# Optimization experiments

Hardware: AMD Instinct MI355X
Metric: run time of the kernel (lower is better)

Reference implementation:

```python
import jax, jax.numpy as jnp
import numpy as np

NTOKEN = 32000
NHID = 1024
BATCH = 64
LEAVES = 256          # leaves per balanced binary tree
SEQLEN = 768          # 3*LEAVES-2 = 766, padded to 768
MAX_DEPTH = 64        # stack bound; balanced tree needs ~log2(LEAVES)+2
OPEN, CLOSE = 0, 1
PAD = NTOKEN - 1


def _build_tree(rng, n_leaves):
    # "( left right )" encoding: open, subtrees, close; leaf ids in [2, NTOKEN-2]
    if n_leaves == 1:
        return [int(rng.integers(2, NTOKEN - 1))]
    l = n_leaves // 2
    return [OPEN] + _build_tree(rng, l) + _build_tree(rng, n_leaves - l) + [CLOSE]


def setup_inputs() -> dict:
    rng = np.random.default_rng(0)
    seqs = []
    for _ in range(BATCH):
        s = _build_tree(rng, LEAVES)
        s = s + [PAD] * (SEQLEN - len(s))
        seqs.append(s)
    tokens = jnp.asarray(np.asarray(seqs, dtype=np.int32).T)  # [S, B]

    key = jax.random.key(0)
    k1, k2 = jax.random.split(key, 2)
    emb = jax.random.normal(k1, (NTOKEN, NHID), jnp.float32) * 0.1
    emb = emb.at[PAD].set(0.0)  # padding_idx row is zero
    W = jax.random.normal(k2, (NHID, 2 * NHID), jnp.float32) * (1.0 / np.sqrt(2 * NHID))
    b = jnp.zeros((NHID,), jnp.float32)
    return {"tokens": tokens, "emb": emb, "W": W, "b": b}


def _parse_all(tokens, emb, W, b):
    # tokens: [S, B] int32. Shift-reduce stack machine, scanned over sequence,
    # vmapped over batch. Dropout is 0 (eval / default), so op = tanh(Linear).
    nhid = emb.shape[1]

    def parse_one(toks):  # toks: [S]
        stack0 = jnp.zeros((MAX_DEPTH, nhid), emb.dtype)

        def step(carry, idx):
            stack, ptr = carry
            is_close = idx == CLOSE
            is_open = idx == OPEN
            is_pad = idx == PAD
            left = stack[ptr - 2]
            right = stack[ptr - 1]
            combined = jnp.tanh(jnp.concatenate([left, right]) @ W.T + b)  # [nhid]
            leaf = emb[idx]
            push = jnp.where(is_close, combined, leaf)
            pos = jnp.where(is_close, ptr - 2, ptr)
            write = jnp.logical_not(is_open | is_pad)
            stack = stack.at[pos].set(jnp.where(write, push, stack[pos]))
            ptr = ptr + jnp.where(is_close, jnp.int32(-1),
                                  jnp.where(write, jnp.int32(1), jnp.int32(0)))
            return (stack, ptr), None

        (stack, _), _ = jax.lax.scan(step, (stack0, jnp.int32(0)), toks)
        return stack[0]  # root representation

    return jax.vmap(parse_one)(tokens.T)  # [B, nhid]


def reference(tokens, emb, W, b):
    return _parse_all(tokens, emb, W, b)
```

## Files before the change

kernel.cpp:

```cpp
#include <hip/hip_runtime.h>

#define B 64
#define SLEN 768
#define NHID 1024
#define K2 2048
#define NTOK 32000
#define PADTOK (NTOK-1)
#define MAXL 16
#define MAXN 256
#define NINT 256
#define NCONV 128
#define LEAFB 2048
#define LEAFROWS (B*SLEN)

typedef unsigned short u16;
typedef unsigned int u32;
typedef __attribute__((ext_vector_type(8))) short short8;
typedef __attribute__((ext_vector_type(4))) float f32x4;

__device__ __forceinline__ u16 f2b(float f) {
  union { float f; u32 i; } v; v.f = f;
  u32 x = v.i;
  return (u16)((x + 0x7FFFu + ((x >> 16) & 1u)) >> 16);
}
__device__ __forceinline__ float fast_tanh(float x) {
  float t = __expf(2.0f * x);
  return 1.0f - 2.0f / (t + 1.0f);
}
__device__ __forceinline__ void glds16(const void* g, void* l) {
  __builtin_amdgcn_global_load_lds(
      (const __attribute__((address_space(1))) void*)g,
      (__attribute__((address_space(3))) void*)l, 16, 0, 0);
}

__launch_bounds__(768)
__global__ void parse_leaf_wconv(const int* __restrict__ tokens,
                                 const float* __restrict__ emb,
                                 const float* __restrict__ W,
                                 int* __restrict__ cnt,
                                 int* __restrict__ rootArr,
                                 int4* __restrict__ nodes,
                                 u16* __restrict__ Wbf,
                                 u16* __restrict__ LeafVals) {
  if (blockIdx.x > NCONV) {
    int base = (blockIdx.x - 1 - NCONV) * 3 + (threadIdx.x >> 8);
    int i = (threadIdx.x & 255) * 4;
    for (int r = base; r < LEAFROWS; r += LEAFB * 3) {
      int b = r / SLEN, t = r - b * SLEN;
      int tok = tokens[t * B + b];
      if (tok < 2 || tok == PADTOK) continue;
      const float* src = emb + (size_t)tok * NHID;
      u16* dst = LeafVals + (size_t)r * NHID;
      float4 v = *reinterpret_cast<const float4*>(src + i);
      ushort4 o = {f2b(v.x), f2b(v.y), f2b(v.z), f2b(v.w)};
      *reinterpret_cast<ushort4*>(dst + i) = o;
    }
    return;
  }
  if (blockIdx.x != 0) {
    int id = (blockIdx.x - 1) * 768 + threadIdx.x;
    int stride = NCONV * 768;
    for (int i = id; i < (NHID * K2) / 4; i += stride) {
      float4 v = reinterpret_cast<const float4*>(W)[i];
      ushort4 o = {f2b(v.x), f2b(v.y), f2b(v.z), f2b(v.w)};
      reinterpret_cast<ushort4*>(Wbf)[i] = o;
    }
    return;
  }

  __shared__ int tok[SLEN];
  __shared__ int SC[SLEN];
  __shared__ short A[16 * SLEN];
  __shared__ int cntLoc[MAXL];

  int t = threadIdx.x;
  tok[t] = tokens[t * B + 0];
  if (t < MAXL) cntLoc[t] = 0;
  __syncthreads();

  int tk = tok[t];
  bool isO = (tk == 0), isC = (tk == 1);
  bool isL = !isO && !isC && (tk != PADTOK);
  int delta = isO ? 1 : (isC ? -1 : 0);
  SC[t] = (delta << 20) + ((isL ? 1 : 0) << 10) + (isC ? 1 : 0);
  __syncthreads();

  for (int off = 1; off < SLEN; off <<= 1) {
    int v = SC[t];
    int u = (t >= off) ? SC[t - off] : 0;
    __syncthreads();
    SC[t] = v + u;
    __syncthreads();
  }

  int S = SC[t];
  int depth = S >> 20; if (depth > 15) depth = 15;
  int clIdx = S & 1023;

#pragma unroll
  for (int d = 0; d < 16; ++d) A[d * SLEN + t] = (depth == d) ? (short)t : (short)-1;
  __syncthreads();
  for (int off = 1; off < SLEN; off <<= 1) {
    short vv[16];
#pragma unroll
    for (int d = 0; d < 16; ++d) {
      short a = A[d * SLEN + t];
      if (t >= off) { short b2 = A[d * SLEN + t - off]; a = (a > b2) ? a : b2; }
      vv[d] = a;
    }
    __syncthreads();
#pragma unroll
    for (int d = 0; d < 16; ++d) A[d * SLEN + t] = vv[d];
    __syncthreads();
  }

  int myid = -1, lref = 0, rref = 0, lce = -1;
  bool rIsLeaf = false, lIsLeaf = false;
  if (isC && t >= 3) {
    myid = clIdx - 1;
    int tm1 = tok[t - 1];
    rIsLeaf = (tm1 != 1);
    rref = rIsLeaf ? (0x40000000 | (t - 1)) : ((SC[t - 1] & 1023) - 1);
    int dd = depth + 1; if (dd > 15) dd = 15;
    lce = rIsLeaf ? (t - 2) : (int)A[dd * SLEN + (t - 2)];
    if (lce >= 0) {
      lIsLeaf = (tok[lce] != 1);
      lref = lIsLeaf ? (0x40000000 | lce) : ((SC[lce] & 1023) - 1);
    }
  }
  __syncthreads();

  short* lvl = A;
  lvl[t] = isC ? (short)1 : (short)0;
  __syncthreads();
  int lv = 1;
  for (int it = 0; it < 15; ++it) {
    if (myid >= 0) {
      int ll = lIsLeaf ? 0 : (int)lvl[lce];
      int rr = rIsLeaf ? 0 : (int)lvl[t - 1];
      lv = (ll > rr ? ll : rr) + 1;
    }
    __syncthreads();
    if (myid >= 0) lvl[t] = (short)lv;
    __syncthreads();
  }
  if (lv > 15) lv = 15;

  if (myid >= 0 && myid < NINT) {
    int slot = atomicAdd(&cntLoc[lv], 1);
    if (slot < MAXN)
      nodes[lv * MAXN + slot] = make_int4(lref, rref, myid, 0);
  }
  __syncthreads();

  if (t == 0) {
    int ncount = SC[SLEN - 1] & 1023;
    rootArr[0] = (ncount > 0) ? (ncount - 1 < NINT ? ncount - 1 : NINT - 1)
                              : 0x40000000;
  }
  if (t >= 1 && t < MAXL) cnt[t] = (cntLoc[t] < MAXN) ? cntLoc[t] : MAXN;
}

template<int LVL>
__launch_bounds__(256, 2)
__global__ void combine_lv(const u16* __restrict__ Wbf,
                           const float* __restrict__ bias,
                           const int* __restrict__ cnt,
                           const int4* __restrict__ nodes,
                           const int* __restrict__ rootArr,
                           const u16* __restrict__ LeafVals,
                           u16* __restrict__ Vals,
                           float* __restrict__ out,
                           const int* __restrict__ tokens,
                           const float* __restrict__ emb) {
  __shared__ short As[4][4096];
  __shared__ short Bs[4][4096];
  __shared__ const u16* sL[128];
  __shared__ const u16* sR[128];
  __shared__ int sOut[128];
  __shared__ int sRoot[128];

  int rootId = rootArr[0];
  if (rootId & 0x40000000) {
    if constexpr (LVL == 1) {
      int pos = rootId & 0xFFFF;
      for (int b = blockIdx.x; b < B; b += gridDim.x) {
        int tokv = tokens[pos * B + b];
        for (int i = threadIdx.x; i < NHID; i += 256)
          out[(size_t)b * NHID + i] = emb[(size_t)tokv * NHID + i];
      }
    }
    return;
  }

  int cnt0 = cnt[LVL];
  if (cnt0 <= 0) return;
  int rowsTotal = B * cnt0;
  int mTiles = (rowsTotal + 127) >> 7;
  int totalTiles = mTiles * 8;
  int tid = threadIdx.x;
  int lane = tid & 63, wave = tid >> 6;
  int wm = wave & 1, wn = wave >> 1;

  for (int tile = blockIdx.x; tile < totalTiles; tile += gridDim.x) {
    int mt = tile >> 3, nt = tile & 7;
    int m0 = mt << 7, n0 = nt << 7;
    __syncthreads();
    if (tid < 128) {
      int r = m0 + tid;
      const u16* lp = Wbf; const u16* rp = Wbf; int ov = -1, rf = -1;
      if (r < rowsTotal) {
        int bb = r / cnt0, j = r - bb * cnt0;
        int4 rec = nodes[LVL * MAXN + j];
        int lr = rec.x, rr = rec.y;
        lp = (lr & 0x40000000) ? LeafVals + (size_t)(bb * SLEN + (lr & 0xFFFF)) * NHID
                               : Vals + ((size_t)bb * NINT + lr) * NHID;
        rp = (rr & 0x40000000) ? LeafVals + (size_t)(bb * SLEN + (rr & 0xFFFF)) * NHID
                               : Vals + ((size_t)bb * NINT + rr) * NHID;
        ov = bb * NINT + rec.z;
        if (rec.z == rootId) rf = bb * NHID;
      }
      sL[tid] = lp; sR[tid] = rp; sOut[tid] = ov; sRoot[tid] = rf;
    }
    __syncthreads();

    int kq = (tid & 3) * 8;
    const u16* a0L = sL[tid >> 2] + kq;        const u16* a0R = sR[tid >> 2] + kq;
    const u16* a1L = sL[64 + (tid >> 2)] + kq; const u16* a1R = sR[64 + (tid >> 2)] + kq;
    const u16* b0 = Wbf + (size_t)(n0 + (tid >> 2)) * K2 + kq;
    const u16* b1 = Wbf + (size_t)(n0 + 64 + (tid >> 2)) * K2 + kq;

    f32x4 acc[4][4];
#pragma unroll
    for (int i = 0; i < 4; ++i)
#pragma unroll
      for (int j = 0; j < 4; ++j) acc[i][j] = {0.f, 0.f, 0.f, 0.f};

    int aBase = (wm * 64 + (lane & 15)) * 32 + (lane >> 4) * 8;
    int bBase = (wn * 64 + (lane & 15)) * 32 + (lane >> 4) * 8;

    auto STAGE = [&](int buf, int k0) {
      const u16* sa0 = (k0 < NHID) ? (a0L + k0) : (a0R + (k0 - NHID));
      const u16* sa1 = (k0 < NHID) ? (a1L + k0) : (a1R + (k0 - NHID));
      short* Ad = &As[buf][0] + wave * 512;
      short* Bd = &Bs[buf][0] + wave * 512;
      glds16(sa0, Ad);
      glds16(sa1, Ad + 2048);
      glds16(b0 + k0, Bd);
      glds16(b1 + k0, Bd + 2048);
    };
    auto COMPUTE = [&](int buf) {
      short8 af[4], bw[4];
#pragma unroll
      for (int mi = 0; mi < 4; ++mi)
        af[mi] = *reinterpret_cast<const short8*>(&As[buf][0] + aBase + mi * 512);
#pragma unroll
      for (int ni = 0; ni < 4; ++ni)
        bw[ni] = *reinterpret_cast<const short8*>(&Bs[buf][0] + bBase + ni * 512);
#pragma unroll
      for (int mi = 0; mi < 4; ++mi)
#pragma unroll
        for (int ni = 0; ni < 4; ++ni)
          acc[mi][ni] = __builtin_amdgcn_mfma_f32_16x16x32_bf16(
              af[mi], bw[ni], acc[mi][ni], 0, 0, 0);
    };

    STAGE(0, 0); STAGE(1, 32); STAGE(2, 64);
    for (int t = 0; t < 61; ++t) {
      asm volatile("s_waitcnt vmcnt(8)" ::: "memory");
      __builtin_amdgcn_s_barrier();
      STAGE((t + 3) & 3, (t + 3) * 32);
      COMPUTE(t & 3);
    }
    asm volatile("s_waitcnt vmcnt(8)" ::: "memory");
    __builtin_amdgcn_s_barrier();
    COMPUTE(61 & 3);
    asm volatile("s_waitcnt vmcnt(4)" ::: "memory");
    __builtin_amdgcn_s_barrier();
    COMPUTE(62 & 3);
    asm volatile("s_waitcnt vmcnt(0)" ::: "memory");
    __builtin_amdgcn_s_barrier();
    COMPUTE(63 & 3);

#pragma unroll
    for (int ni = 0; ni < 4; ++ni) {
      int n = n0 + wn * 64 + ni * 16 + (lane & 15);
      float bv = bias[n];
#pragma unroll
      for (int mi = 0; mi < 4; ++mi) {
#pragma unroll
        for (int reg = 0; reg < 4; ++reg) {
          int mloc = wm * 64 + mi * 16 + (lane >> 4) * 4 + reg;
          int ov = sOut[mloc];
          if (ov >= 0) {
            float v = fast_tanh(acc[mi][ni][reg] + bv);
            Vals[(size_t)ov * NHID + n] = f2b(v);
            int rf = sRoot[mloc];
            if (rf >= 0) out[rf + n] = v;
          }
        }
      }
    }
  }
}

extern "C" void kernel_launch(void* const* d_in, const int* in_sizes, int n_in,
                              void* d_out, int out_size, void* d_ws, size_t ws_size,
                              hipStream_t stream) {
  const int* tokens = (const int*)d_in[0];
  const float* emb  = (const float*)d_in[1];
  const float* W    = (const float*)d_in[2];
  const float* bias = (const float*)d_in[3];
  float* out = (float*)d_out;

  char* ws = (char*)d_ws;
  int* cnt      = (int*)ws;
  int* rootArr  = (int*)(ws + 4096);
  int4* nodes   = (int4*)(ws + 12288);
  u16* Wbf      = (u16*)(ws + 131072);
  u16* LeafVals = (u16*)(ws + 4325376);
  u16* Vals     = (u16*)(ws + 4325376 + (size_t)B * SLEN * NHID * 2);

  parse_leaf_wconv<<<1 + NCONV + LEAFB, 768, 0, stream>>>(
      tokens, emb, W, cnt, rootArr, nodes, Wbf, LeafVals);

#define LAUNCH_LVL(L)                                                     \
  do {                                                                    \
    int expRows = B * (256 >> (L));                                       \
    int mT = (expRows + 127) / 128;                                       \
    combine_lv<L><<<mT * 8, 256, 0, stream>>>(Wbf, bias, cnt, nodes,      \
        rootArr, LeafVals, Vals, out, tokens, emb);                       \
  } while (0)
  LAUNCH_LVL(1); LAUNCH_LVL(2); LAUNCH_LVL(3); LAUNCH_LVL(4);
  LAUNCH_LVL(5); LAUNCH_LVL(6); LAUNCH_LVL(7); LAUNCH_LVL(8);
#undef LAUNCH_LVL
}
```

Baseline: 639.7 us.

## Pre-pack GEMM operands into swizzled tile layout written directly by parents

Rather than gathering rows from separate leaf and node buffers through per-row pointers, each level's A operand is now stored as contiguous, pre-swizzled 128x32 tiles. Leaf embeddings and combine outputs are scattered straight into their parent's row and column slot, and W is converted into the same tiled swizzled layout. This gives fully contiguous loads with no pointer indirection, no LDS bank conflicts, and no materialization of unused leaf rows. The combine pipeline drops from 4 to 3 LDS buffers to fit 3 blocks per CU. The cost is an extra scatter kernel, strided scattered stores in the epilogue, and more complex parse bookkeeping.

Result: slower. 699.1 us (+9.3%).

```diff
diff --git a/kernel.cpp b/kernel.cpp
--- a/kernel.cpp
+++ b/kernel.cpp
@@ -10,8 +10,6 @@
 #define MAXN 256
 #define NINT 256
 #define NCONV 128
-#define LEAFB 2048
-#define LEAFROWS (B*SLEN)
 
 typedef unsigned short u16;
 typedef unsigned int u32;
@@ -33,37 +31,31 @@
       (__attribute__((address_space(3))) void*)l, 16, 0, 0);
 }
 
+__device__ __forceinline__ size_t swz(int row, int col) {
+  return ((size_t)((row >> 7) * 64 + (col >> 5)) << 12)
+       + (size_t)(((row & 127) << 5)
+       + (((((col >> 3) & 3) ^ ((row >> 1) & 3))) << 3)
+       + (col & 7));
+}
+
 __launch_bounds__(768)
-__global__ void parse_leaf_wconv(const int* __restrict__ tokens,
-                                 const float* __restrict__ emb,
-                                 const float* __restrict__ W,
-                                 int* __restrict__ cnt,
-                                 int* __restrict__ rootArr,
-                                 int4* __restrict__ nodes,
-                                 u16* __restrict__ Wbf,
-                                 u16* __restrict__ LeafVals) {
-  if (blockIdx.x > NCONV) {
-    int base = (blockIdx.x - 1 - NCONV) * 3 + (threadIdx.x >> 8);
-    int i = (threadIdx.x & 255) * 4;
-    for (int r = base; r < LEAFROWS; r += LEAFB * 3) {
-      int b = r / SLEN, t = r - b * SLEN;
-      int tok = tokens[t * B + b];
-      if (tok < 2 || tok == PADTOK) continue;
-      const float* src = emb + (size_t)tok * NHID;
-      u16* dst = LeafVals + (size_t)r * NHID;
-      float4 v = *reinterpret_cast<const float4*>(src + i);
-      ushort4 o = {f2b(v.x), f2b(v.y), f2b(v.z), f2b(v.w)};
-      *reinterpret_cast<ushort4*>(dst + i) = o;
-    }
-    return;
-  }
+__global__ void parse_wt(const int* __restrict__ tokens,
+                         const float* __restrict__ W,
+                         int* __restrict__ cnt,
+                         int* __restrict__ aoffG,
+                         int* __restrict__ rootArr,
+                         int* __restrict__ leafParG,
+                         int* __restrict__ nodeMeta,
+                         u16* __restrict__ Wt) {
   if (blockIdx.x != 0) {
     int id = (blockIdx.x - 1) * 768 + threadIdx.x;
     int stride = NCONV * 768;
     for (int i = id; i < (NHID * K2) / 4; i += stride) {
       float4 v = reinterpret_cast<const float4*>(W)[i];
+      int n = i >> 9;
+      int k = (i << 2) & 2047;
       ushort4 o = {f2b(v.x), f2b(v.y), f2b(v.z), f2b(v.w)};
-      reinterpret_cast<ushort4*>(Wbf)[i] = o;
+      *reinterpret_cast<ushort4*>(Wt + swz(n, k)) = o;
     }
     return;
   }
@@ -72,10 +64,14 @@
   __shared__ int SC[SLEN];
   __shared__ short A[16 * SLEN];
   __shared__ int cntLoc[MAXL];
+  __shared__ int nodePar[NINT];
+  __shared__ int leafPar[SLEN];
 
   int t = threadIdx.x;
   tok[t] = tokens[t * B + 0];
   if (t < MAXL) cntLoc[t] = 0;
+  if (t < NINT) nodePar[t] = -1;
+  leafPar[t] = -1;
   __syncthreads();
 
   int tk = tok[t];
@@ -114,18 +110,17 @@
     __syncthreads();
   }
 
-  int myid = -1, lref = 0, rref = 0, lce = -1;
+  int myid = -1, lce = -1, lNid = -1, rNid = -1;
   bool rIsLeaf = false, lIsLeaf = false;
   if (isC && t >= 3) {
     myid = clIdx - 1;
-    int tm1 = tok[t - 1];
-    rIsLeaf = (tm1 != 1);
-    rref = rIsLeaf ? (0x40000000 | (t - 1)) : ((SC[t - 1] & 1023) - 1);
+    rIsLeaf = (tok[t - 1] != 1);
+    if (!rIsLeaf) rNid = (SC[t - 1] & 1023) - 1;
     int dd = depth + 1; if (dd > 15) dd = 15;
     lce = rIsLeaf ? (t - 2) : (int)A[dd * SLEN + (t - 2)];
     if (lce >= 0) {
       lIsLeaf = (tok[lce] != 1);
-      lref = lIsLeaf ? (0x40000000 | lce) : ((SC[lce] & 1023) - 1);
+      if (!lIsLeaf) lNid = (SC[lce] & 1023) - 1;
     }
   }
   __syncthreads();
@@ -136,7 +131,7 @@
   int lv = 1;
   for (int it = 0; it < 15; ++it) {
     if (myid >= 0) {
-      int ll = lIsLeaf ? 0 : (int)lvl[lce];
+      int ll = lIsLeaf ? 0 : (lce >= 0 ? (int)lvl[lce] : 0);
       int rr = rIsLeaf ? 0 : (int)lvl[t - 1];
       lv = (ll > rr ? ll : rr) + 1;
     }
@@ -146,55 +141,86 @@
   }
   if (lv > 15) lv = 15;
 
-  if (myid >= 0 && myid < NINT) {
-    int slot = atomicAdd(&cntLoc[lv], 1);
-    if (slot < MAXN)
-      nodes[lv * MAXN + slot] = make_int4(lref, rref, myid, 0);
-  }
-  __syncthreads();
+  int slot = -1;
+  if (myid >= 0 && myid < NINT) slot = atomicAdd(&cntLoc[lv], 1);
+  __syncthreads();
+  if (slot >= 0 && slot < MAXN) {
+    int pkL = (lv << 20) | (slot << 4);
+    int pkR = pkL | 1;
+    if (lce >= 0) {
+      if (lIsLeaf) leafPar[lce] = pkL;
+      else if (lNid >= 0 && lNid < NINT) nodePar[lNid] = pkL;
+    }
+    if (rIsLeaf) leafPar[t - 1] = pkR;
+    else if (rNid >= 0 && rNid < NINT) nodePar[rNid] = pkR;
+  }
+  __syncthreads();
+  if (slot >= 0 && slot < MAXN)
+    nodeMeta[lv * MAXN + slot] = nodePar[myid];
+  leafParG[t] = leafPar[t];
 
   if (t == 0) {
     int ncount = SC[SLEN - 1] & 1023;
-    rootArr[0] = (ncount > 0) ? (ncount - 1 < NINT ? ncount - 1 : NINT - 1)
-                              : 0x40000000;
-  }
-  if (t >= 1 && t < MAXL) cnt[t] = (cntLoc[t] < MAXN) ? cntLoc[t] : MAXN;
+    rootArr[0] = (ncount > 0) ? 0 : 0x40000000;
+    int run = 0;
+    for (int l = 1; l < MAXL; ++l) {
+      int c = cntLoc[l] < MAXN ? cntLoc[l] : MAXN;
+      cnt[l] = c;
+      aoffG[l] = run;
+      run += (B * c + 127) & ~127;
+    }
+  }
+}
+
+__global__ void leaf_scatter(const int* __restrict__ tokens,
+                             const float* __restrict__ emb,
+                             const int* __restrict__ leafPar,
+                             const int* __restrict__ cnt,
+                             const int* __restrict__ aoff,
+                             const int* __restrict__ rootArr,
+                             u16* __restrict__ Apack,
+                             float* __restrict__ out) {
+  int i4 = threadIdx.x * 4;
+  bool deg = (rootArr[0] & 0x40000000) != 0;
+  for (int r = blockIdx.x; r < B * SLEN; r += gridDim.x) {
+    int b = r / SLEN, pos = r - b * SLEN;
+    if (deg) {
+      if (pos == 0) {
+        int tk = tokens[0 * B + b];
+        float4 v = *reinterpret_cast<const float4*>(emb + (size_t)tk * NHID + i4);
+        *reinterpret_cast<float4*>(out + (size_t)b * NHID + i4) = v;
+      }
+      continue;
+    }
+    int pk = leafPar[pos];
+    if (pk < 0) continue;
+    int tk = tokens[pos * B + b];
+    int lvP = pk >> 20, sP = (pk >> 4) & 0xFFFF, side = pk & 1;
+    int prow = aoff[lvP] + b * cnt[lvP] + sP;
+    int col = (side << 10) + i4;
+    float4 v = *reinterpret_cast<const float4*>(emb + (size_t)tk * NHID + i4);
+    ushort4 o = {f2b(v.x), f2b(v.y), f2b(v.z), f2b(v.w)};
+    *reinterpret_cast<ushort4*>(Apack + swz(prow, col)) = o;
+  }
 }
 
 template<int LVL>
-__launch_bounds__(256, 2)
-__global__ void combine_lv(const u16* __restrict__ Wbf,
+__launch_bounds__(256, 3)
+__global__ void combine_lv(const u16* __restrict__ Wt,
                            const float* __restrict__ bias,
                            const int* __restrict__ cnt,
-                           const int4* __restrict__ nodes,
-                           const int* __restrict__ rootArr,
-                           const u16* __restrict__ LeafVals,
-                           u16* __restrict__ Vals,
-                           float* __restrict__ out,
-                           const int* __restrict__ tokens,
-                           const float* __restrict__ emb) {
-  __shared__ short As[4][4096];
-  __shared__ short Bs[4][4096];
-  __shared__ const u16* sL[128];
-  __shared__ const u16* sR[128];
-  __shared__ int sOut[128];
-  __shared__ int sRoot[128];
-
-  int rootId = rootArr[0];
-  if (rootId & 0x40000000) {
-    if constexpr (LVL == 1) {
-      int pos = rootId & 0xFFFF;
-      for (int b = blockIdx.x; b < B; b += gridDim.x) {
-        int tokv = tokens[pos * B + b];
-        for (int i = threadIdx.x; i < NHID; i += 256)
-          out[(size_t)b * NHID + i] = emb[(size_t)tokv * NHID + i];
-      }
-    }
-    return;
-  }
+                           const int* __restrict__ aoff,
+                           const int* __restrict__ nodeMeta,
+                           u16* __restrict__ Apack,
+                           float* __restrict__ out) {
+  __shared__ short As[3][4096];
+  __shared__ short Bs[3][4096];
+  __shared__ int sPr[128];
+  __shared__ int sCs[128];
 
   int cnt0 = cnt[LVL];
   if (cnt0 <= 0) return;
+  int aoffL = aoff[LVL];
   int rowsTotal = B * cnt0;
   int mTiles = (rowsTotal + 127) >> 7;
   int totalTiles = mTiles * 8;
@@ -208,27 +234,24 @@
     __syncthreads();
     if (tid < 128) {
       int r = m0 + tid;
-      const u16* lp = Wbf; const u16* rp = Wbf; int ov = -1, rf = -1;
+      int pr = -2, cs = 0;
       if (r < rowsTotal) {
         int bb = r / cnt0, j = r - bb * cnt0;
-        int4 rec = nodes[LVL * MAXN + j];
-        int lr = rec.x, rr = rec.y;
-        lp = (lr & 0x40000000) ? LeafVals + (size_t)(bb * SLEN + (lr & 0xFFFF)) * NHID
-                               : Vals + ((size_t)bb * NINT + lr) * NHID;
-        rp = (rr & 0x40000000) ? LeafVals + (size_t)(bb * SLEN + (rr & 0xFFFF)) * NHID
-                               : Vals + ((size_t)bb * NINT + rr) * NHID;
-        ov = bb * NINT + rec.z;
-        if (rec.z == rootId) rf = bb * NHID;
-      }
-      sL[tid] = lp; sR[tid] = rp; sOut[tid] = ov; sRoot[tid] = rf;
-    }
-    __syncthreads();
-
-    int kq = (tid & 3) * 8;
-    const u16* a0L = sL[tid >> 2] + kq;        const u16* a0R = sR[tid >> 2] + kq;
-    const u16* a1L = sL[64 + (tid >> 2)] + kq; const u16* a1R = sR[64 + (tid >> 2)] + kq;
-    const u16* b0 = Wbf + (size_t)(n0 + (tid >> 2)) * K2 + kq;
-    const u16* b1 = Wbf + (size_t)(n0 + 64 + (tid >> 2)) * K2 + kq;
+        int meta = nodeMeta[LVL * MAXN + j];
+        if (meta < 0) { pr = -1; cs = bb * NHID; }
+        else {
+          int lvP = meta >> 20, sP = (meta >> 4) & 0xFFFF, side = meta & 1;
+          pr = aoff[lvP] + bb * cnt[lvP] + sP;
+          cs = side << 10;
+        }
+      }
+      sPr[tid] = pr; sCs[tid] = cs;
+    }
+    __syncthreads();
+
+    const u16* Ab = Apack + ((size_t)(((aoffL + m0) >> 7) * 64) << 12);
+    const u16* Bb = Wt + ((size_t)((n0 >> 7) * 64) << 12);
+    int lofs = wave * 512 + lane * 8;
 
     f32x4 acc[4][4];
 #pragma unroll
@@ -236,27 +259,31 @@
 #pragma unroll
       for (int j = 0; j < 4; ++j) acc[i][j] = {0.f, 0.f, 0.f, 0.f};
 
-    int aBase = (wm * 64 + (lane & 15)) * 32 + (lane >> 4) * 8;
-    int bBase = (wn * 64 + (lane & 15)) * 32 + (lane >> 4) * 8;
-
-    auto STAGE = [&](int buf, int k0) {
-      const u16* sa0 = (k0 < NHID) ? (a0L + k0) : (a0R + (k0 - NHID));
-      const u16* sa1 = (k0 < NHID) ? (a1L + k0) : (a1R + (k0 - NHID));
+    auto STAGE = [&](int buf, int kc) {
+      const u16* sa = Ab + ((size_t)kc << 12) + lofs;
+      const u16* sb = Bb + ((size_t)kc << 12) + lofs;
       short* Ad = &As[buf][0] + wave * 512;
       short* Bd = &Bs[buf][0] + wave * 512;
-      glds16(sa0, Ad);
-      glds16(sa1, Ad + 2048);
-      glds16(b0 + k0, Bd);
-      glds16(b1 + k0, Bd + 2048);
+      glds16(sa, Ad);
+      glds16(sa + 2048, Ad + 2048);
+      glds16(sb, Bd);
+      glds16(sb + 2048, Bd + 2048);
     };
     auto COMPUTE = [&](int buf) {
       short8 af[4], bw[4];
-#pragma unroll
-      for (int mi = 0; mi < 4; ++mi)
-        af[mi] = *reinterpret_cast<const short8*>(&As[buf][0] + aBase + mi * 512);
-#pragma unroll
-      for (int ni = 0; ni < 4; ++ni)
-        bw[ni] = *reinterpret_cast<const short8*>(&Bs[buf][0] + bBase + ni * 512);
+      int q = lane >> 4;
+#pragma unroll
+      for (int mi = 0; mi < 4; ++mi) {
+        int rA = wm * 64 + mi * 16 + (lane & 15);
+        af[mi] = *reinterpret_cast<const short8*>(
+            &As[buf][(rA << 5) + ((q ^ ((rA >> 1) & 3)) << 3)]);
+      }
+#pragma unroll
+      for (int ni = 0; ni < 4; ++ni) {
+        int rB = wn * 64 + ni * 16 + (lane & 15);
+        bw[ni] = *reinterpret_cast<const short8*>(
+            &Bs[buf][(rB << 5) + ((q ^ ((rB >> 1) & 3)) << 3)]);
+      }
 #pragma unroll
       for (int mi = 0; mi < 4; ++mi)
 #pragma unroll
@@ -265,22 +292,23 @@
               af[mi], bw[ni], acc[mi][ni], 0, 0, 0);
     };
 
-    STAGE(0, 0); STAGE(1, 32); STAGE(2, 64);
-    for (int t = 0; t < 61; ++t) {
-      asm volatile("s_waitcnt vmcnt(8)" ::: "memory");
+    STAGE(0, 0); STAGE(1, 1);
+    int bc = 0, bs = 2;
+    for (int t = 0; t < 62; ++t) {
+      asm volatile("s_waitcnt vmcnt(4)" ::: "memory");
       __builtin_amdgcn_s_barrier();
-      STAGE((t + 3) & 3, (t + 3) * 32);
-      COMPUTE(t & 3);
-    }
-    asm volatile("s_waitcnt vmcnt(8)" ::: "memory");
-    __builtin_amdgcn_s_barrier();
-    COMPUTE(61 & 3);
+      STAGE(bs, t + 2);
+      COMPUTE(bc);
+      bc = (bc == 2) ? 0 : bc + 1;
+      bs = (bs == 2) ? 0 : bs + 1;
+    }
     asm volatile("s_waitcnt vmcnt(4)" ::: "memory");
     __builtin_amdgcn_s_barrier();
-    COMPUTE(62 & 3);
+    COMPUTE(bc);
+    bc = (bc == 2) ? 0 : bc + 1;
     asm volatile("s_waitcnt vmcnt(0)" ::: "memory");
     __builtin_amdgcn_s_barrier();
-    COMPUTE(63 & 3);
+    COMPUTE(bc);
 
 #pragma unroll
     for (int ni = 0; ni < 4; ++ni) {
@@ -291,12 +319,11 @@
 #pragma unroll
         for (int reg = 0; reg < 4; ++reg) {
           int mloc = wm * 64 + mi * 16 + (lane >> 4) * 4 + reg;
-          int ov = sOut[mloc];
-          if (ov >= 0) {
+          int pr = sPr[mloc];
+          if (pr != -2) {
             float v = fast_tanh(acc[mi][ni][reg] + bv);
-            Vals[(size_t)ov * NHID + n] = f2b(v);
-            int rf = sRoot[mloc];
-            if (rf >= 0) out[rf + n] = v;
+            if (pr == -1) out[sCs[mloc] + n] = v;
+            else Apack[swz(pr, sCs[mloc] + n)] = f2b(v);
           }
         }
       }
@@ -316,20 +343,24 @@
   char* ws = (char*)d_ws;
   int* cnt      = (int*)ws;
   int* rootArr  = (int*)(ws + 4096);
-  int4* nodes   = (int4*)(ws + 12288);
-  u16* Wbf      = (u16*)(ws + 131072);
-  u16* LeafVals = (u16*)(ws + 4325376);
-  u16* Vals     = (u16*)(ws + 4325376 + (size_t)B * SLEN * NHID * 2);
-
-  parse_leaf_wconv<<<1 + NCONV + LEAFB, 768, 0, stream>>>(
-      tokens, emb, W, cnt, rootArr, nodes, Wbf, LeafVals);
+  int* aoff     = (int*)(ws + 8192);
+  int* leafPar  = (int*)(ws + 12288);
+  int* nodeMeta = (int*)(ws + 16384);
+  u16* Wt       = (u16*)(ws + 65536);
+  u16* Apack    = (u16*)(ws + 4259840);
+
+  parse_wt<<<1 + NCONV, 768, 0, stream>>>(tokens, W, cnt, aoff, rootArr,
+                                          leafPar, nodeMeta, Wt);
+
+  leaf_scatter<<<4096, 256, 0, stream>>>(tokens, emb, leafPar, cnt, aoff,
+                                         rootArr, Apack, out);
 
 #define LAUNCH_LVL(L)                                                     \
   do {                                                                    \
     int expRows = B * (256 >> (L));                                       \
     int mT = (expRows + 127) / 128;                                       \
-    combine_lv<L><<<mT * 8, 256, 0, stream>>>(Wbf, bias, cnt, nodes,      \
-        rootArr, LeafVals, Vals, out, tokens, emb);                       \
+    combine_lv<L><<<mT * 8, 256, 0, stream>>>(Wt, bias, cnt, aoff,        \
+                                              nodeMeta, Apack, out);      \
   } while (0)
   LAUNCH_LVL(1); LAUNCH_LVL(2); LAUNCH_LVL(3); LAUNCH_LVL(4);
   LAUNCH_LVL(5); LAUNCH_LVL(6); LAUNCH_LVL(7); LAUNCH_LVL(8);
```
